# Kernel optimization log

Measured on AMD Instinct MI355X. Metric: run time of the kernel, lower is better.

## Reference

```python
import jax, jax.numpy as jnp
import numpy as np

B, K, V = 8192, 1024, 2


def setup_inputs() -> dict:
    key = jax.random.key(0)
    k1, k2, k3, k4, k5, k6 = jax.random.split(key, 6)
    z = jax.random.normal(k1, (B, K), dtype=jnp.float32)
    # -1 means no intervention for that sample
    intervention_target = jax.random.randint(k2, (B,), -1, K)
    intervention_variant = jax.random.randint(k3, (B,), 0, V)
    raw_adjacency = jax.random.normal(k4, (K, K), dtype=jnp.float32) * 0.05
    intervention_means = jax.random.normal(k5, (K, V), dtype=jnp.float32)
    intervention_log_scales = jax.random.normal(k6, (K, V), dtype=jnp.float32) * 0.1
    return {
        "z": z,
        "intervention_target": intervention_target,
        "intervention_variant": intervention_variant,
        "raw_adjacency": raw_adjacency,
        "intervention_means": intervention_means,
        "intervention_log_scales": intervention_log_scales,
    }


def _scm_forward(z, target, variant, raw_adjacency, means, log_scales):
    Kd = z.shape[1]
    # strictly-lower-triangular adjacency (row j holds parents of node j)
    A = raw_adjacency * jnp.tril(jnp.ones((Kd, Kd), z.dtype), k=-1)

    def step(u, xs):
        a_row, mean_row, logsc_row, z_j, j = xs
        # forward substitution: u_j = z_j + sum_{i<j} A[j,i] * u_i
        # columns >= j of u are still zero and A row is zero there too
        value = z_j + u @ a_row  # [B]
        # intervention overwrite for samples with target == j
        m = mean_row[variant]                 # [B]
        s = jnp.exp(logsc_row[variant])       # [B]
        value = jnp.where(target == j, m + s * z_j, value)
        u = jax.lax.dynamic_update_slice(u, value[:, None], (0, j))
        return u, None

    u0 = jnp.zeros_like(z)
    xs = (A, means, log_scales, z.T, jnp.arange(Kd))
    u, _ = jax.lax.scan(step, u0, xs)
    return u


def reference(z, intervention_target, intervention_variant, raw_adjacency,
              intervention_means, intervention_log_scales):
    return _scm_forward(z, intervention_target, intervention_variant,
                        raw_adjacency, intervention_means, intervention_log_scales)
```

## Files before the change

### kernel.cpp

```cpp
#include <hip/hip_runtime.h>
#include <hip/hip_bf16.h>
#include <cstdint>

#define KDIM 1024
#define BDIM 8192
#define VDIM 2
#define NBLK 16

#if defined(__has_builtin)
#if __has_builtin(__builtin_amdgcn_global_load_lds)
#define HAS_GLL 1
#endif
#endif
#ifndef HAS_GLL
#define HAS_GLL 0
#endif

typedef __attribute__((ext_vector_type(8))) short short8;
typedef __attribute__((ext_vector_type(4))) float f32x4;

__device__ inline unsigned short f2bf(float x) {
  unsigned u = __builtin_bit_cast(unsigned, x);
  u = (u + 0x7FFFu + ((u >> 16) & 1u)) >> 16;
  return (unsigned short)u;
}

__device__ inline float bf2f(unsigned short x) {
  return __builtin_bit_cast(float, (unsigned)x << 16);
}


#define STAGE_T(DST, SRC, ROW0, COL0, LD)                                   \
  {                                                                         \
    const float* _s = (SRC);                                                \
    _Pragma("unroll") for (int _p = 0; _p < 4; ++_p) {                      \
      const int _m = _p * 16 + rw;                                          \
      float4 _v = *(const float4*)(_s + (size_t)((ROW0) + _m) * (LD) +      \
                                   (COL0) + 4 * k4);                        \
      (DST)[4 * k4 + 0][_m] = _v.x;                                         \
      (DST)[4 * k4 + 1][_m] = _v.y;                                         \
      (DST)[4 * k4 + 2][_m] = _v.z;                                         \
      (DST)[4 * k4 + 3][_m] = _v.w;                                         \
    }                                                                       \
  }

#define STAGE_D(DST, SRC, ROW0, COL0, LD)                                   \
  {                                                                         \
    const float* _s = (SRC);                                                \
    _Pragma("unroll") for (int _p = 0; _p < 4; ++_p) {                      \
      const int _kk = _p * 16 + rw;                                         \
      *(float4*)&(DST)[_kk][4 * k4] =                                       \
          *(const float4*)(_s + (size_t)((ROW0) + _kk) * (LD) + (COL0) +    \
                           4 * k4);                                         \
    }                                                                       \
  }

#define ZERO_ACC                                                            \
  _Pragma("unroll") for (int _a = 0; _a < 4; ++_a)                          \
      _Pragma("unroll") for (int _b = 0; _b < 4; ++_b) acc[_a][_b] = 0.f;

__device__ __forceinline__ void mac64(const float (*Ls)[68],
                                      const float (*Rs)[68], int tm, int tn,
                                      float acc[4][4]) {
#pragma unroll 4
  for (int k = 0; k < 64; ++k) {
    const float4 av = *(const float4*)&Ls[k][4 * tm];
    const float4 bv = *(const float4*)&Rs[k][4 * tn];
    const float aa[4] = {av.x, av.y, av.z, av.w};
    const float bb4[4] = {bv.x, bv.y, bv.z, bv.w};
#pragma unroll
    for (int a = 0; a < 4; ++a)
#pragma unroll
      for (int b = 0; b < 4; ++b) acc[a][b] += aa[a] * bb4[b];
  }
}

#define STORE_MT(R0, C0)                                                    \
  _Pragma("unroll") for (int _a = 0; _a < 4; ++_a) {                        \
    *(float4*)(MT + (size_t)((R0) + 4 * tm + _a) * KDIM + (C0) + 4 * tn) =  \
        make_float4(acc[_a][0], acc[_a][1], acc[_a][2], acc[_a][3]);        \
  }

#define MBF_TILE(R0, C0, BUF)                                               \
  {                                                                         \
    __syncthreads();                                                        \
    _Pragma("unroll") for (int _a = 0; _a < 4; ++_a)                        \
        _Pragma("unroll") for (int _b = 0; _b < 4; ++_b)                    \
            (BUF)[4 * tm + _a][4 * tn + _b] = acc[_a][_b];                  \
    __syncthreads();                                                        \
    const int _tr = tid >> 4, _tc = tid & 15;                               \
    _Pragma("unroll") for (int _p = 0; _p < 4; ++_p) {                      \
      const int _il = _p * 16 + _tr;                                        \
      ushort4 _o;                                                           \
      _o.x = f2bf((BUF)[4 * _tc + 0][_il]);                                 \
      _o.y = f2bf((BUF)[4 * _tc + 1][_il]);                                 \
      _o.z = f2bf((BUF)[4 * _tc + 2][_il]);                                 \
      _o.w = f2bf((BUF)[4 * _tc + 3][_il]);                                 \
      *(ushort4*)(Mbf + (size_t)((C0) + _il) * KDIM + (R0) + 4 * _tc) = _o; \
    }                                                                       \
  }

__global__ __launch_bounds__(256) void comb01(const float* __restrict__ A,
                                              float* __restrict__ MT,
                                              unsigned short* __restrict__ Mbf) {
  int b = blockIdx.x;
  const int rt = b & 1;
  const int jt = (b >> 1) & 1;
  const int s = b >> 2;
  const int base = s * 256;

  __shared__ float shpool[6 * 64 * 68];
  float (*Ls)[68] = (float(*)[68])(shpool);
  float (*Rs)[68] = (float(*)[68])(shpool + 4352);
  float (*tQ0L)[68] = (float(*)[68])(shpool + 2 * 4352);
  float (*tQ0H)[68] = (float(*)[68])(shpool + 3 * 4352);
  float (*tP0)[68] = (float(*)[68])(shpool + 4 * 4352);
  float (*tP1)[68] = (float(*)[68])(shpool + 5 * 4352);
  float* As4 = shpool + 2 * 4352;

  const int tid = threadIdx.x;
  const int k4 = tid & 15;
  const int rw = tid >> 4;
  const int tm = tid >> 4;
  const int tn = tid & 15;
  float acc[4][4];

  {
    const int g = tid >> 6;
    const int c = tid & 63;
    const int dbase = base + g * 64;
    float* Asg = As4 + g * 4096;
    for (int r = 0; r < 64; ++r)
      Asg[r * 64 + c] = A[(size_t)(dbase + r) * KDIM + dbase + c];
    __syncthreads();
    float m[64];
#pragma unroll
    for (int r = 0; r < 64; ++r) m[r] = (r == c) ? 1.f : 0.f;
#pragma unroll
    for (int r = 1; r < 64; ++r) {
      float a0 = 0.f, a1 = 0.f;
#pragma unroll
      for (int i = 0; i < 64; ++i) {
        if (i >= r) break;
        if (i & 1) a1 += Asg[r * 64 + i] * m[i];
        else       a0 += Asg[r * 64 + i] * m[i];
      }
      const float v = a0 + a1;
      m[r] = (r > c) ? v : m[r];
    }
#pragma unroll
    for (int r = 0; r < 64; r += 4)
      *(float4*)(MT + (size_t)(dbase + c) * KDIM + dbase + r) =
          make_float4(m[r], m[r + 1], m[r + 2], m[r + 3]);
    if (jt == 0 && rt == 0) {
#pragma unroll
      for (int r = 0; r < 64; ++r)
        Mbf[(size_t)(dbase + r) * KDIM + dbase + c] = f2bf(m[r]);
    }
    __syncthreads();
  }

  if (jt == 0) {
    STAGE_T(Ls, MT, base, base, KDIM);
    STAGE_T(Rs, A, base + 64, base, KDIM);
    __syncthreads();
    ZERO_ACC;
    mac64(Ls, Rs, tm, tn, acc);
    __syncthreads();
#pragma unroll
    for (int a = 0; a < 4; ++a)
#pragma unroll
      for (int b2 = 0; b2 < 4; ++b2) tP0[4 * tn + b2][4 * tm + a] = acc[a][b2];
    STAGE_D(Rs, MT, base + 64, base + 64, KDIM);
    __syncthreads();
    ZERO_ACC;
    mac64(tP0, Rs, tm, tn, acc);
    __syncthreads();
#pragma unroll
    for (int a = 0; a < 4; ++a)
#pragma unroll
      for (int b2 = 0; b2 < 4; ++b2) tQ0L[4 * tn + b2][4 * tm + a] = acc[a][b2];
    if (rt == 0) {
      STORE_MT(base, base + 64);
      MBF_TILE(base, base + 64, Rs);
    }
  }
  __syncthreads();

  if (rt == 1) {
    STAGE_T(Ls, MT, base + 128, base + 128, KDIM);
    STAGE_T(Rs, A, base + 192, base + 128, KDIM);
    __syncthreads();
    ZERO_ACC;
    mac64(Ls, Rs, tm, tn, acc);
    __syncthreads();
#pragma unroll
    for (int a = 0; a < 4; ++a)
#pragma unroll
      for (int b2 = 0; b2 < 4; ++b2) tP1[4 * tn + b2][4 * tm + a] = acc[a][b2];
    STAGE_D(Rs, MT, base + 192, base + 192, KDIM);
    __syncthreads();
    ZERO_ACC;
    mac64(tP1, Rs, tm, tn, acc);
    __syncthreads();
#pragma unroll
    for (int a = 0; a < 4; ++a)
#pragma unroll
      for (int b2 = 0; b2 < 4; ++b2) tQ0H[4 * tm + a][4 * tn + b2] = acc[a][b2];
    if (jt == 1) {
      STORE_MT(base + 128, base + 192);
      MBF_TILE(base + 128, base + 192, Rs);
    }
  }
  __syncthreads();

  STAGE_T(Ls, MT, base + 64 * jt, base + 64 * jt, KDIM);
  __syncthreads();
  for (int kb2 = 0; kb2 <= rt; ++kb2) {
    ZERO_ACC;
    for (int kb = jt; kb < 2; ++kb) {
      STAGE_T(Rs, A, base + 128 + 64 * kb2, base + 64 * kb, KDIM);
      __syncthreads();
      mac64(kb == jt ? Ls : tQ0L, Rs, tm, tn, acc);
      __syncthreads();
    }
    if (kb2 == 0) {
#pragma unroll
      for (int a = 0; a < 4; ++a)
#pragma unroll
        for (int b2 = 0; b2 < 4; ++b2) tP0[4 * tn + b2][4 * tm + a] = acc[a][b2];
    } else {
#pragma unroll
      for (int a = 0; a < 4; ++a)
#pragma unroll
        for (int b2 = 0; b2 < 4; ++b2) tP1[4 * tn + b2][4 * tm + a] = acc[a][b2];
    }
  }
  __syncthreads();

  ZERO_ACC;
  if (rt == 0) {
    STAGE_D(Rs, MT, base + 128, base + 128, KDIM);
    __syncthreads();
    mac64(tP0, Rs, tm, tn, acc);
    __syncthreads();
  } else {
    mac64(tP0, tQ0H, tm, tn, acc);
    __syncthreads();
    STAGE_D(Rs, MT, base + 192, base + 192, KDIM);
    __syncthreads();
    mac64(tP1, Rs, tm, tn, acc);
    __syncthreads();
  }
  STORE_MT(base + 64 * jt, base + 128 + 64 * rt);
  MBF_TILE(base + 64 * jt, base + 128 + 64 * rt, Rs);
}

__global__ __launch_bounds__(256) void p4_stream(
    const float* __restrict__ A, float* __restrict__ MT,
    float* __restrict__ Pt, const float* __restrict__ Z,
    unsigned short* __restrict__ Zbf, unsigned short* __restrict__ Mbf,
    int do_zbf) {
  __shared__ float Ls[64][68];
  __shared__ float Rs[64][68];

  if (blockIdx.x >= 32) {
    const int wid = blockIdx.x - 32;
    const int nw = gridDim.x - 32;
    const int idx0 = wid * 256 + threadIdx.x;
    const int stride = nw * 256;
    const float4 z4 = make_float4(0.f, 0.f, 0.f, 0.f);
    const uint4 u4 = make_uint4(0u, 0u, 0u, 0u);

    for (int i = idx0; i < 256 * 1024; i += stride) {
      const int blk = i >> 10, off = i & 1023;
      const int bi = blk >> 4, bj = blk & 15;
      if (bi <= bj) continue;
      *(float4*)(MT + (size_t)(bi * 64 + (off >> 4)) * KDIM + bj * 64 +
                 4 * (off & 15)) = z4;
    }
    for (int i = idx0; i < 256 * 512; i += stride) {
      const int blk = i >> 9, off = i & 511;
      const int bi = blk >> 4, bj = blk & 15;
      if (bi >= bj) continue;
      *(uint4*)(Mbf + (size_t)(bi * 64 + (off >> 3)) * KDIM + bj * 64 +
                8 * (off & 7)) = u4;
    }
    if (do_zbf) {
      for (int i = idx0; i < BDIM * KDIM / 4; i += stride) {
        float4 v = *(const float4*)(Z + 4 * (size_t)i);
        ushort4 o;
        o.x = f2bf(v.x);
        o.y = f2bf(v.y);
        o.z = f2bf(v.z);
        o.w = f2bf(v.w);
        *(ushort4*)(Zbf + 4 * (size_t)i) = o;
      }
    }
    return;
  }

  int b = blockIdx.x;
  const int T = 4;
  const int rb = b % T; b /= T;
  const int jb = b % T; b /= T;
  const int c = b;
  const int h = 64 * T;
  const int base = c * 2 * h;

  const int tid = threadIdx.x;
  const int k4 = tid & 15;
  const int rw = tid >> 4;
  const int tm = tid >> 4;
  const int tn = tid & 15;
  float acc[4][4];
  ZERO_ACC;

  for (int kb = jb; kb < T; ++kb) {
    STAGE_T(Ls, MT, base + 64 * jb, base + 64 * kb, KDIM);
    STAGE_T(Rs, A, base + h + 64 * rb, base + 64 * kb, KDIM);
    __syncthreads();
    mac64(Ls, Rs, tm, tn, acc);
    __syncthreads();
  }

  float* P0 = Pt + (size_t)c * h * h;
#pragma unroll
  for (int a = 0; a < 4; ++a)
    *(float4*)(P0 + (size_t)(64 * jb + 4 * tm + a) * h + 64 * rb + 4 * tn) =
        make_float4(acc[a][0], acc[a][1], acc[a][2], acc[a][3]);
}

template <int T>
__global__ __launch_bounds__(256) void p_k(const float* __restrict__ A,
                                           const float* __restrict__ MT,
                                           float* __restrict__ Pt) {
  int b = blockIdx.x;
  const int rb = b % T; b /= T;
  const int jb = b % T; b /= T;
  const int c = b;
  const int h = 64 * T;
  const int base = c * 2 * h;

  __shared__ float Ls[64][68];
  __shared__ float Rs[64][68];
  const int tid = threadIdx.x;
  const int k4 = tid & 15;
  const int rw = tid >> 4;
  const int tm = tid >> 4;
  const int tn = tid & 15;
  float acc[4][4];
  ZERO_ACC;

  for (int kb = jb; kb < T; ++kb) {
    STAGE_T(Ls, MT, base + 64 * jb, base + 64 * kb, KDIM);
    STAGE_T(Rs, A, base + h + 64 * rb, base + 64 * kb, KDIM);
    __syncthreads();
    mac64(Ls, Rs, tm, tn, acc);
    __syncthreads();
  }

  float* P0 = Pt + (size_t)c * h * h;
#pragma unroll
  for (int a = 0; a < 4; ++a)
    *(float4*)(P0 + (size_t)(64 * jb + 4 * tm + a) * h + 64 * rb + 4 * tn) =
        make_float4(acc[a][0], acc[a][1], acc[a][2], acc[a][3]);
}

template <int T>
__global__ __launch_bounds__(256) void q_k(float* __restrict__ MT,
                                           const float* __restrict__ Pt,
                                           unsigned short* __restrict__ Mbf) {
  int b = blockIdx.x;
  const int rb = b % T; b /= T;
  const int jb = b % T; b /= T;
  const int c = b;
  const int h = 64 * T;
  const int base = c * 2 * h;

  __shared__ float Ls[64][68];
  __shared__ float Rs[64][68];
  const int tid = threadIdx.x;
  const int k4 = tid & 15;
  const int rw = tid >> 4;
  const int tm = tid >> 4;
  const int tn = tid & 15;
  float acc[4][4];
  ZERO_ACC;

  const float* P0 = Pt + (size_t)c * h * h;
  for (int kb = 0; kb <= rb; ++kb) {
    STAGE_T(Ls, P0, 64 * jb, 64 * kb, h);
    STAGE_D(Rs, MT, base + h + 64 * kb, base + h + 64 * rb, KDIM);
    __syncthreads();
    mac64(Ls, Rs, tm, tn, acc);
    __syncthreads();
  }

  STORE_MT(base + 64 * jb, base + h + 64 * rb);
  MBF_TILE(base + 64 * jb, base + h + 64 * rb, Ls);
}

#define LDB 72

template <int ZBF>
__global__ __launch_bounds__(256) void gemm_mfma(
    const float* __restrict__ Z, const unsigned short* __restrict__ Zbf,
    const unsigned short* __restrict__ Mbf, const float* __restrict__ MT,
    const int* __restrict__ tgt, const int* __restrict__ var,
    const float* __restrict__ means, const float* __restrict__ lsc,
    float* __restrict__ C) {
  __shared__ unsigned short As[128][LDB];
#if HAS_GLL
  __shared__ unsigned short Bs[128][64];
#else
  __shared__ unsigned short Bs[128][LDB];
#endif
  __shared__ float scoef[128];
  __shared__ int stb[128];

  const int d = blockIdx.x;
  const int xbl = d & 7;
  const int nir = (d >> 3) & 7;
  const int xbh = d >> 6;
  const int xb = xbh * 8 + xbl;
  const int ni = (xb & 32) ? (7 - nir) : nir;
  const int b0 = xb * 128;
  const int i0 = ni * 128;

  const int tid = threadIdx.x;
  const int w = tid >> 6;
  const int lane = tid & 63;
  const int wr = w >> 1, wc = w & 1;
  const int mlane = lane & 15;
  const int q = lane >> 4;

  const int rq = tid >> 4, kq = tid & 15;
  const int cb = tid >> 3, ck = tid & 7;

  f32x4 acc[4][4];
#pragma unroll
  for (int a = 0; a < 4; ++a)
#pragma unroll
    for (int b = 0; b < 4; ++b) acc[a][b] = (f32x4){0.f, 0.f, 0.f, 0.f};

  const int nkb = 2 * (ni + 1);
  for (int kb = 0; kb < nkb; ++kb) {
    const int k0 = kb * 64;
    if (ZBF) {
#pragma unroll
      for (int p = 0; p < 4; ++p) {
        const int r = p * 32 + cb;
        *(uint4*)&As[r][8 * ck] =
            *(const uint4*)(Zbf + (size_t)(b0 + r) * KDIM + k0 + 8 * ck);
      }
    } else {
#pragma unroll
      for (int p = 0; p < 8; ++p) {
        const int r = p * 16 + rq;
        float4 zv = *(const float4*)(Z + (size_t)(b0 + r) * KDIM + k0 + 4 * kq);
        ushort4 o;
        o.x = f2bf(zv.x);
        o.y = f2bf(zv.y);
        o.z = f2bf(zv.z);
        o.w = f2bf(zv.w);
        *(ushort4*)&As[r][4 * kq] = o;
      }
    }
#if HAS_GLL
    {
      const int rl = lane >> 3;
      const int ch = lane & 7;
#pragma unroll
      for (int i = 0; i < 4; ++i) {
        const int row = w * 32 + i * 8 + rl;
        const int sch = ch ^ (row & 7);
        const unsigned short* src =
            Mbf + (size_t)(i0 + row) * KDIM + k0 + sch * 8;
        __builtin_amdgcn_global_load_lds(
            (const __attribute__((address_space(1))) void*)src,
            (__attribute__((address_space(3))) void*)&Bs[w * 32 + i * 8][0],
            16, 0, 0);
      }
    }
#else
#pragma unroll
    for (int p = 0; p < 4; ++p) {
      const int c = p * 32 + cb;
      *(uint4*)&Bs[c][8 * ck] =
          *(const uint4*)(Mbf + (size_t)(i0 + c) * KDIM + k0 + 8 * ck);
    }
#endif
    __syncthreads();
#pragma unroll
    for (int ks = 0; ks < 2; ++ks) {
      const int kf = ks * 32 + q * 8;
      short8 av[4], bv[4];
#pragma unroll
      for (int a = 0; a < 4; ++a)
        av[a] = *(const short8*)&As[wr * 64 + 16 * a + mlane][kf];
#if HAS_GLL
      const char* BsB = (const char*)&Bs[0][0];
#pragma unroll
      for (int b = 0; b < 4; ++b) {
        const int row = wc * 64 + 16 * b + mlane;
        bv[b] = *(const short8*)(BsB + row * 128 +
                                 ((2 * kf) ^ ((row & 7) << 4)));
      }
#else
#pragma unroll
      for (int b = 0; b < 4; ++b)
        bv[b] = *(const short8*)&Bs[wc * 64 + 16 * b + mlane][kf];
#endif
#pragma unroll
      for (int a = 0; a < 4; ++a)
#pragma unroll
        for (int b = 0; b < 4; ++b)
          acc[a][b] =
              __builtin_amdgcn_mfma_f32_16x16x32_bf16(av[a], bv[b], acc[a][b], 0, 0, 0);
    }
    __syncthreads();
  }

  {
    const int s = tid >> 1, h2 = tid & 1;
    const int br = b0 + s;
    const int tb = tgt[br];
    float part = 0.f;
    if (tb >= 0) {
      const int nk16 = (tb >> 4) + 1;
      if (ZBF) {
        const unsigned short* zr = Zbf + (size_t)br * KDIM;
        const unsigned short* mr = Mbf + (size_t)tb * KDIM;
        for (int c16 = h2; c16 < nk16; c16 += 2) {
          const uint4 za = *(const uint4*)(zr + c16 * 16);
          const uint4 zb2 = *(const uint4*)(zr + c16 * 16 + 8);
          const uint4 ma = *(const uint4*)(mr + c16 * 16);
          const uint4 mb2 = *(const uint4*)(mr + c16 * 16 + 8);
          const unsigned zw[8] = {za.x, za.y, za.z, za.w,
                                  zb2.x, zb2.y, zb2.z, zb2.w};
          const unsigned mw[8] = {ma.x, ma.y, ma.z, ma.w,
                                  mb2.x, mb2.y, mb2.z, mb2.w};
#pragma unroll
          for (int wv = 0; wv < 8; ++wv) {
            part += __builtin_bit_cast(float, zw[wv] << 16) *
                    __builtin_bit_cast(float, mw[wv] << 16);
            part += __builtin_bit_cast(float, zw[wv] & 0xFFFF0000u) *
                    __builtin_bit_cast(float, mw[wv] & 0xFFFF0000u);
          }
        }
      } else {
        const float* zr = Z + (size_t)br * KDIM;
        const unsigned short* mr = Mbf + (size_t)tb * KDIM;
        const int nk8 = (tb >> 3) + 1;
        for (int c8 = h2; c8 < nk8; c8 += 2) {
          const float4 z0 = *(const float4*)(zr + c8 * 8);
          const float4 z1 = *(const float4*)(zr + c8 * 8 + 4);
          const ushort4 m0 = *(const ushort4*)(mr + c8 * 8);
          const ushort4 m1 = *(const ushort4*)(mr + c8 * 8 + 4);
          part += z0.x * bf2f(m0.x) + z0.y * bf2f(m0.y) + z0.z * bf2f(m0.z) +
                  z0.w * bf2f(m0.w) + z1.x * bf2f(m1.x) + z1.y * bf2f(m1.y) +
                  z1.z * bf2f(m1.z) + z1.w * bf2f(m1.w);
        }
      }
    }
    part += __shfl_down(part, 1);
    if (h2 == 0) {
      float cf = 0.f;
      int tbs = 0;
      if (tb >= 0) {
        const int v = var[br];
        const float mval = means[tb * VDIM + v];
        const float sval = expf(lsc[tb * VDIM + v]);
        const float zv = Z[(size_t)br * KDIM + tb];
        cf = (mval + sval * zv) - part;
        tbs = tb;
      }
      scoef[s] = cf;
      stb[s] = tbs;
    }
  }
  __syncthreads();

#pragma unroll
  for (int a = 0; a < 4; ++a) {
    const int l0 = wr * 64 + 16 * a + q * 4;
    const int row0 = b0 + l0;
#pragma unroll
    for (int b = 0; b < 4; ++b) {
      const int col = i0 + wc * 64 + 16 * b + mlane;
      float* Cp = C + (size_t)row0 * KDIM + col;
#pragma unroll
      for (int j = 0; j < 4; ++j) {
        const float cf = scoef[l0 + j];
        const float corr = cf * MT[(size_t)stb[l0 + j] * KDIM + col];
        Cp[j * KDIM] = acc[a][b][j] + corr;
      }
    }
  }
}

extern "C" void kernel_launch(void* const* d_in, const int* in_sizes, int n_in,
                              void* d_out, int out_size, void* d_ws,
                              size_t ws_size, hipStream_t stream) {
  const float* z = (const float*)d_in[0];
  const int* tgt = (const int*)d_in[1];
  const int* var = (const int*)d_in[2];
  const float* A = (const float*)d_in[3];
  const float* means = (const float*)d_in[4];
  const float* lsc = (const float*)d_in[5];
  float* out = (float*)d_out;

  char* ws = (char*)d_ws;
  float* MT = (float*)ws;
  unsigned short* Mbf = (unsigned short*)(ws + (4u << 20));
  float* Pt2 = (float*)(ws + (6u << 20));
  float* Pt3 = (float*)(ws + (6u << 20) + (512u << 10));
  unsigned short* Zbf = (unsigned short*)(ws + (7u << 20) + (512u << 10));
  const int use_zbf =
      ws_size >= (7u << 20) + (512u << 10) + (size_t)BDIM * KDIM * 2 ? 1 : 0;

  hipLaunchKernelGGL(comb01, dim3(16), dim3(256), 0, stream, A, MT, Mbf);
  hipLaunchKernelGGL(p4_stream, dim3(512), dim3(256), 0, stream, A, MT, Pt2, z,
                     Zbf, Mbf, use_zbf);
  hipLaunchKernelGGL((q_k<4>), dim3(32), dim3(256), 0, stream, MT, Pt2, Mbf);
  hipLaunchKernelGGL((p_k<8>), dim3(64), dim3(256), 0, stream, A, MT, Pt3);
  hipLaunchKernelGGL((q_k<8>), dim3(64), dim3(256), 0, stream, MT, Pt3, Mbf);
  if (use_zbf)
    hipLaunchKernelGGL((gemm_mfma<1>), dim3((BDIM / 128) * (KDIM / 128)),
                       dim3(256), 0, stream, z, Zbf, Mbf, MT, tgt, var, means,
                       lsc, out);
  else
    hipLaunchKernelGGL((gemm_mfma<0>), dim3((BDIM / 128) * (KDIM / 128)),
                       dim3(256), 0, stream, z, Zbf, Mbf, MT, tgt, var, means,
                       lsc, out);
}
```

Baseline: 244.1 us.

## Invert 64x64 diagonal blocks via two 32x32 inversions plus block GEMM

The per-thread serial 64-row forward substitution for each 64x64 diagonal block inverse is replaced by a recursive scheme. Two 32x32 triangular inverses are computed in parallel, and the off-diagonal block is formed with two small register-tiled GEMMs in shared memory. Padded strides (65/33) are used to reduce LDS bank conflicts. This shortens the serial dependency chain and cuts register pressure from 64 to 32 floats per thread, at the cost of extra syncs and float4 loads from odd-stride arrays that may be misaligned.

```diff
diff --git a/kernel.cpp b/kernel.cpp
--- a/kernel.cpp
+++ b/kernel.cpp
@@ -116,7 +116,6 @@
   float (*tQ0H)[68] = (float(*)[68])(shpool + 3 * 4352);
   float (*tP0)[68] = (float(*)[68])(shpool + 4 * 4352);
   float (*tP1)[68] = (float(*)[68])(shpool + 5 * 4352);
-  float* As4 = shpool + 2 * 4352;
 
   const int tid = threadIdx.x;
   const int k4 = tid & 15;
@@ -126,36 +125,142 @@
   float acc[4][4];
 
   {
+    float* Tt = shpool;
+    float* As4 = shpool + 2 * 4352;
     const int g = tid >> 6;
-    const int c = tid & 63;
+    const int l = tid & 63;
     const int dbase = base + g * 64;
-    float* Asg = As4 + g * 4096;
+    float* Asg = As4 + g * 4160;
+
     for (int r = 0; r < 64; ++r)
-      Asg[r * 64 + c] = A[(size_t)(dbase + r) * KDIM + dbase + c];
-    __syncthreads();
-    float m[64];
-#pragma unroll
-    for (int r = 0; r < 64; ++r) m[r] = (r == c) ? 1.f : 0.f;
-#pragma unroll
-    for (int r = 1; r < 64; ++r) {
-      float a0 = 0.f, a1 = 0.f;
-#pragma unroll
-      for (int i = 0; i < 64; ++i) {
-        if (i >= r) break;
-        if (i & 1) a1 += Asg[r * 64 + i] * m[i];
-        else       a0 += Asg[r * 64 + i] * m[i];
-      }
-      const float v = a0 + a1;
-      m[r] = (r > c) ? v : m[r];
-    }
-#pragma unroll
-    for (int r = 0; r < 64; r += 4)
-      *(float4*)(MT + (size_t)(dbase + c) * KDIM + dbase + r) =
-          make_float4(m[r], m[r + 1], m[r + 2], m[r + 3]);
-    if (jt == 0 && rt == 0) {
-#pragma unroll
-      for (int r = 0; r < 64; ++r)
-        Mbf[(size_t)(dbase + r) * KDIM + dbase + c] = f2bf(m[r]);
+      Asg[r * 65 + l] = A[(size_t)(dbase + r) * KDIM + dbase + l];
+    __syncthreads();
+
+    {
+      const int h = l >> 5, c = l & 31;
+      const float* Ah = Asg + (32 * h) * 65 + 32 * h;
+      float m[32];
+#pragma unroll
+      for (int r = 0; r < 32; ++r) m[r] = (r == c) ? 1.f : 0.f;
+#pragma unroll
+      for (int r = 1; r < 32; ++r) {
+        float a0 = 0.f, a1 = 0.f;
+#pragma unroll
+        for (int i = 0; i < 32; ++i) {
+          if (i >= r) break;
+          if (i & 1) a1 += Ah[r * 65 + i] * m[i];
+          else       a0 += Ah[r * 65 + i] * m[i];
+        }
+        const float v = a0 + a1;
+        m[r] = (r > c) ? v : m[r];
+      }
+      float* Th = Tt + g * 2112 + h * 1056;
+#pragma unroll
+      for (int r = 0; r < 32; ++r) Th[r * 33 + c] = m[r];
+    }
+    __syncthreads();
+
+    const int tm8 = l >> 3, tn8 = l & 7;
+    {
+      float u[4][4];
+#pragma unroll
+      for (int a = 0; a < 4; ++a)
+#pragma unroll
+        for (int b2 = 0; b2 < 4; ++b2) u[a][b2] = 0.f;
+      const float* T1 = Tt + g * 2112;
+#pragma unroll
+      for (int ki = 0; ki < 8; ++ki) {
+        float4 av[4], bv[4];
+#pragma unroll
+        for (int a = 0; a < 4; ++a)
+          av[a] = *(const float4*)&Asg[(32 + 4 * tm8 + a) * 65 + 4 * ki];
+#pragma unroll
+        for (int j = 0; j < 4; ++j)
+          bv[j] = *(const float4*)&T1[(4 * ki + j) * 33 + 4 * tn8];
+#pragma unroll
+        for (int a = 0; a < 4; ++a) {
+          const float aa[4] = {av[a].x, av[a].y, av[a].z, av[a].w};
+#pragma unroll
+          for (int j = 0; j < 4; ++j) {
+            const float bb[4] = {bv[j].x, bv[j].y, bv[j].z, bv[j].w};
+#pragma unroll
+            for (int b2 = 0; b2 < 4; ++b2) u[a][b2] += aa[j] * bb[b2];
+          }
+        }
+      }
+#pragma unroll
+      for (int a = 0; a < 4; ++a)
+#pragma unroll
+        for (int b2 = 0; b2 < 4; ++b2)
+          Asg[(4 * tm8 + a) * 32 + 4 * tn8 + b2] = u[a][b2];
+    }
+    __syncthreads();
+
+    {
+      float t21[4][4];
+#pragma unroll
+      for (int a = 0; a < 4; ++a)
+#pragma unroll
+        for (int b2 = 0; b2 < 4; ++b2) t21[a][b2] = 0.f;
+      const float* T2 = Tt + g * 2112 + 1056;
+#pragma unroll
+      for (int ki = 0; ki < 8; ++ki) {
+        float4 av[4], bv[4];
+#pragma unroll
+        for (int a = 0; a < 4; ++a)
+          av[a] = *(const float4*)&T2[(4 * tm8 + a) * 33 + 4 * ki];
+#pragma unroll
+        for (int j = 0; j < 4; ++j)
+          bv[j] = *(const float4*)&Asg[(4 * ki + j) * 32 + 4 * tn8];
+#pragma unroll
+        for (int a = 0; a < 4; ++a) {
+          const float aa[4] = {av[a].x, av[a].y, av[a].z, av[a].w};
+#pragma unroll
+          for (int j = 0; j < 4; ++j) {
+            const float bb[4] = {bv[j].x, bv[j].y, bv[j].z, bv[j].w};
+#pragma unroll
+            for (int b2 = 0; b2 < 4; ++b2) t21[a][b2] += aa[j] * bb[b2];
+          }
+        }
+      }
+#pragma unroll
+      for (int a = 0; a < 4; ++a)
+#pragma unroll
+        for (int b2 = 0; b2 < 4; ++b2)
+          Asg[1024 + (4 * tm8 + a) * 32 + 4 * tn8 + b2] = t21[a][b2];
+    }
+    __syncthreads();
+
+    {
+      const float* T21 = Asg + 1024;
+      const float* Tg = Tt + g * 2112;
+      for (int r4 = 0; r4 < 16; ++r4) {
+        float vals[4];
+#pragma unroll
+        for (int j = 0; j < 4; ++j) {
+          const int r = 4 * r4 + j;
+          float v;
+          if (r < 32)
+            v = (l < 32) ? Tg[r * 33 + l] : 0.f;
+          else
+            v = (l < 32) ? T21[(r - 32) * 32 + l]
+                         : Tg[1056 + (r - 32) * 33 + (l - 32)];
+          vals[j] = v;
+        }
+        *(float4*)(MT + (size_t)(dbase + l) * KDIM + dbase + 4 * r4) =
+            make_float4(vals[0], vals[1], vals[2], vals[3]);
+      }
+      if (jt == 0 && rt == 0) {
+        for (int r = 0; r < 64; ++r) {
+          float v;
+          if (r < 32)
+            v = (l < 32) ? Tg[r * 33 + l] : 0.f;
+          else
+            v = (l < 32) ? T21[(r - 32) * 32 + l]
+                         : Tg[1056 + (r - 32) * 33 + (l - 32)];
+          Mbf[(size_t)(dbase + r) * KDIM + dbase + l] = f2bf(v);
+        }
+      }
     }
     __syncthreads();
   }
```

New measurement: 246.2 us. About the same (+0.9%).
